# Kernel optimization log

Hardware: AMD Instinct MI355X
Metric: run time of the kernel (lower is better)

Reference implementation:

```python
import jax, jax.numpy as jnp
import numpy as np

N = 4096

def setup_inputs() -> dict:
    key = jax.random.key(0)
    kA, kB = jax.random.split(key)
    A = jnp.tril(jax.random.normal(kA, (N, N), dtype=jnp.float32))
    B = jnp.tril(jax.random.normal(kB, (N, N), dtype=jnp.float32))
    return {"A": A, "B": B}

def reference(A, B):
    # Product of two lower-triangular matrices; result is lower-triangular.
    # tril applied to the dense matmul reproduces the intended math exactly
    # (and zeroes any numerical noise in the structural-zero upper triangle).
    return jnp.tril(jnp.matmul(A, B))
```

## Files before the change

### kernel.cpp

```cpp
#include <hip/hip_runtime.h>
#include <stdint.h>

#define NN 4096
#define NB 32
#define BK 32

#define NHEAVY 136
#define NHUNITS 272
#define ZBASE 664
#define TGRID 1160

#define PGRID 8328

typedef __bf16 bf16x8 __attribute__((ext_vector_type(8)));
typedef float f32x4 __attribute__((ext_vector_type(4)));
typedef unsigned short ushort8 __attribute__((ext_vector_type(8)));

__device__ __forceinline__ unsigned short f2bf(float x) {
    union { float f; unsigned int u; } v; v.f = x;
    unsigned int u = v.u;
    u += 0x7fffu + ((u >> 16) & 1u);
    return (unsigned short)(u >> 16);
}

#define GLOAD16(g, l) __builtin_amdgcn_global_load_lds( \
    (const __attribute__((address_space(1))) unsigned int*)(g), \
    (__attribute__((address_space(3))) unsigned int*)(l), 16, 0, 0)

__device__ __forceinline__ void heavy_map(int h, int& bi, int& bj) {
    int t = h, d = NB - 1;
    while (t >= NB - d) { t -= NB - d; --d; }
    bj = t; bi = t + d;
}

__global__ __launch_bounds__(256) void prep(const float* __restrict__ A,
                                            const float* __restrict__ B,
                                            unsigned short* __restrict__ Ab,
                                            unsigned short* __restrict__ Bt,
                                            float* __restrict__ C) {
    __shared__ float tile[64][65];
    int bid = blockIdx.x;
    int tid = threadIdx.x;

    if (bid < 4096) {
        int i = bid;
        int nslots = (((i >> 7) + 1) * 128) >> 3;
        const float4* src = reinterpret_cast<const float4*>(A + (size_t)i * NN);
        unsigned short* dst = Ab + (size_t)i * NN;
        for (int p = tid; p < nslots; p += 256) {
            float4 x0 = src[p * 2], x1 = src[p * 2 + 1];
            ushort8 o;
            o[0] = f2bf(x0.x); o[1] = f2bf(x0.y); o[2] = f2bf(x0.z); o[3] = f2bf(x0.w);
            o[4] = f2bf(x1.x); o[5] = f2bf(x1.y); o[6] = f2bf(x1.z); o[7] = f2bf(x1.w);
            *reinterpret_cast<ushort8*>(dst + p * 8) = o;
        }
        return;
    }
    if (bid < 8192) {
        int s = bid - 4096;
        int n64 = s >> 6, k64 = s & 63;
        if (k64 < (n64 & ~1)) return;
        int n0 = n64 * 64, k0 = k64 * 64;
        int tx = tid & 63, ty = tid >> 6;
#pragma unroll
        for (int r = 0; r < 16; ++r) {
            int k = ty + r * 4;
            tile[k][tx] = B[(size_t)(k0 + k) * NN + n0 + tx];
        }
        __syncthreads();
#pragma unroll
        for (int r = 0; r < 16; ++r) {
            int n = ty + r * 4;
            Bt[(size_t)(n0 + n) * NN + k0 + tx] = f2bf(tile[tx][n]);
        }
        return;
    }
    int h = bid - 8192;
    int bi, bj; heavy_map(h, bi, bj);
    float4 z = make_float4(0.f, 0.f, 0.f, 0.f);
    float4* cp = reinterpret_cast<float4*>(C + (size_t)bi * 128 * NN + (size_t)bj * 128);
#pragma unroll
    for (int i2 = 0; i2 < 16; ++i2) {
        int slot = tid + i2 * 256;
        int row = slot >> 5, c4 = slot & 31;
        cp[(size_t)row * (NN / 4) + c4] = z;
    }
}

__global__ __launch_bounds__(256) void trimm(const unsigned short* __restrict__ Ab,
                                             const unsigned short* __restrict__ Bt,
                                             float* __restrict__ C) {
    int bid = blockIdx.x;
    int tid = threadIdx.x;
    int lane = tid & 63;
    int w = tid >> 6;

    int bi, bj;
    bool heavy = false;
    int k_lo, k_hi;

    if (bid >= ZBASE) {
        int t = bid - ZBASE;
        int r = 0, cnt = NB - 1;
        while (t >= cnt) { t -= cnt; ++r; --cnt; }
        bi = r; bj = r + 1 + t;
        float4 z = make_float4(0.f, 0.f, 0.f, 0.f);
        float4* cp = reinterpret_cast<float4*>(C + (size_t)bi * 128 * NN + (size_t)bj * 128);
#pragma unroll
        for (int i2 = 0; i2 < 16; ++i2) {
            int slot = tid + i2 * 256;
            int row = slot >> 5, c4 = slot & 31;
            cp[(size_t)row * (NN / 4) + c4] = z;
        }
        return;
    }
    if (bid < NHUNITS) {
        heavy = true;
        int h = bid >> 1, half = bid & 1;
        heavy_map(h, bi, bj);
        k_lo = bj * 128;
        k_hi = (bi + 1) * 128;
        int len = (k_hi - k_lo) >> 1;
        if (half == 0) k_hi = k_lo + len;
        else           k_lo = k_lo + len;
    } else {
        int t = bid - NHUNITS, d = 15;
        while (t >= NB - d) { t -= NB - d; --d; }
        bj = t; bi = t + d;
        k_lo = bj * 128;
        k_hi = (bi + 1) * 128;
    }

    __shared__ unsigned short As[2][128 * BK];
    __shared__ unsigned short Bs[2][128 * BK];

    int wr = w >> 1, wc = w & 1;

    int srow = w * 32 + (lane >> 2);
    int skoff = (lane & 3) * 8;
    const unsigned short* gA0 = Ab + (size_t)(bi * 128 + srow) * NN + skoff;
    const unsigned short* gA1 = gA0 + (size_t)16 * NN;
    const unsigned short* gB0 = Bt + (size_t)(bj * 128 + srow) * NN + skoff;
    const unsigned short* gB1 = gB0 + (size_t)16 * NN;

    f32x4 acc[4][4];
#pragma unroll
    for (int mi = 0; mi < 4; ++mi)
#pragma unroll
        for (int ni = 0; ni < 4; ++ni)
            acc[mi][ni] = (f32x4){0.f, 0.f, 0.f, 0.f};

    int arow = wr * 64 + (lane & 15);
    int brow = wc * 64 + (lane & 15);
    int kq = (lane >> 4) * 8;

    {
        unsigned short* a = &As[0][w * 1024];
        unsigned short* b = &Bs[0][w * 1024];
        GLOAD16(gA0 + k_lo, a);
        GLOAD16(gA1 + k_lo, a + 512);
        GLOAD16(gB0 + k_lo, b);
        GLOAD16(gB1 + k_lo, b + 512);
    }
    int cur = 0;

    for (int kt = k_lo; kt < k_hi; kt += BK) {
        __syncthreads();

        if (kt + BK < k_hi) {
            unsigned short* a = &As[cur ^ 1][w * 1024];
            unsigned short* b = &Bs[cur ^ 1][w * 1024];
            GLOAD16(gA0 + kt + BK, a);
            GLOAD16(gA1 + kt + BK, a + 512);
            GLOAD16(gB0 + kt + BK, b);
            GLOAD16(gB1 + kt + BK, b + 512);
        }

        bf16x8 af[4], bfr[4];
#pragma unroll
        for (int mi = 0; mi < 4; ++mi)
            af[mi] = *reinterpret_cast<const bf16x8*>(&As[cur][(arow + mi * 16) * BK + kq]);
#pragma unroll
        for (int ni = 0; ni < 4; ++ni)
            bfr[ni] = *reinterpret_cast<const bf16x8*>(&Bs[cur][(brow + ni * 16) * BK + kq]);
#pragma unroll
        for (int mi = 0; mi < 4; ++mi)
#pragma unroll
            for (int ni = 0; ni < 4; ++ni)
                acc[mi][ni] = __builtin_amdgcn_mfma_f32_16x16x32_bf16(af[mi], bfr[ni], acc[mi][ni], 0, 0, 0);

        cur ^= 1;
    }

    int crow0 = bi * 128 + wr * 64 + (lane >> 4) * 4;
    int ccol0 = bj * 128 + wc * 64 + (lane & 15);
    if (heavy) {
#pragma unroll
        for (int mi = 0; mi < 4; ++mi)
#pragma unroll
            for (int ni = 0; ni < 4; ++ni) {
                float* cp = C + (size_t)(crow0 + mi * 16) * NN + ccol0 + ni * 16;
#pragma unroll
                for (int r2 = 0; r2 < 4; ++r2)
                    atomicAdd(&cp[(size_t)r2 * NN], acc[mi][ni][r2]);
            }
    } else {
#pragma unroll
        for (int mi = 0; mi < 4; ++mi)
#pragma unroll
            for (int ni = 0; ni < 4; ++ni) {
                float* cp = C + (size_t)(crow0 + mi * 16) * NN + ccol0 + ni * 16;
#pragma unroll
                for (int r2 = 0; r2 < 4; ++r2)
                    cp[(size_t)r2 * NN] = acc[mi][ni][r2];
            }
    }
}

extern "C" void kernel_launch(void* const* d_in, const int* in_sizes, int n_in,
                              void* d_out, int out_size, void* d_ws, size_t ws_size,
                              hipStream_t stream) {
    const float* A = (const float*)d_in[0];
    const float* B = (const float*)d_in[1];
    float* C = (float*)d_out;
    unsigned short* Ab = (unsigned short*)d_ws;
    unsigned short* Bt = Ab + (size_t)NN * NN;
    prep<<<PGRID, 256, 0, stream>>>(A, B, Ab, Bt, C);
    trimm<<<TGRID, 256, 0, stream>>>(Ab, Bt, C);
}
```

Before: 85.86 us.

## Split every lower tile's K range into 512-wide chunks with atomic accumulation

Replaces the two-way split of only the heaviest tiles with a uniform split-K scheme. Each lower-triangular 128x128 output tile's K range is cut into chunks of at most 512, giving 1704 work units of bounded length. Tiles that need several chunks are zeroed in prep and accumulated with atomics, while single-chunk tiles store directly. This evens out per-block work and fills the GPU better, at the cost of many more atomic adds and more zeroing of C in prep.

```diff
diff --git a/kernel.cpp b/kernel.cpp
--- a/kernel.cpp
+++ b/kernel.cpp
@@ -5,12 +5,12 @@
 #define NB 32
 #define BK 32
 
-#define NHEAVY 136
-#define NHUNITS 272
-#define ZBASE 664
-#define TGRID 1160
-
-#define PGRID 8328
+#define NUNITS 1704
+#define ZBASE 1704
+#define TGRID 2200
+
+#define NMULTI 406
+#define PGRID 8598
 
 typedef __bf16 bf16x8 __attribute__((ext_vector_type(8)));
 typedef float f32x4 __attribute__((ext_vector_type(4)));
@@ -26,12 +26,6 @@
 #define GLOAD16(g, l) __builtin_amdgcn_global_load_lds( \
     (const __attribute__((address_space(1))) unsigned int*)(g), \
     (__attribute__((address_space(3))) unsigned int*)(l), 16, 0, 0)
-
-__device__ __forceinline__ void heavy_map(int h, int& bi, int& bj) {
-    int t = h, d = NB - 1;
-    while (t >= NB - d) { t -= NB - d; --d; }
-    bj = t; bi = t + d;
-}
 
 __global__ __launch_bounds__(256) void prep(const float* __restrict__ A,
                                             const float* __restrict__ B,
@@ -75,15 +69,22 @@
         }
         return;
     }
-    int h = bid - 8192;
-    int bi, bj; heavy_map(h, bi, bj);
-    float4 z = make_float4(0.f, 0.f, 0.f, 0.f);
-    float4* cp = reinterpret_cast<float4*>(C + (size_t)bi * 128 * NN + (size_t)bj * 128);
-#pragma unroll
-    for (int i2 = 0; i2 < 16; ++i2) {
-        int slot = tid + i2 * 256;
-        int row = slot >> 5, c4 = slot & 31;
-        cp[(size_t)row * (NN / 4) + c4] = z;
+    {
+        int z = bid - 8192;
+        int d = 31, bi, bj;
+        for (;;) {
+            int cnt = NB - d;
+            if (z < cnt) { bj = z; bi = z + d; break; }
+            z -= cnt; --d;
+        }
+        float4 zf = make_float4(0.f, 0.f, 0.f, 0.f);
+        float4* cp = reinterpret_cast<float4*>(C + (size_t)bi * 128 * NN + (size_t)bj * 128);
+#pragma unroll
+        for (int i2 = 0; i2 < 16; ++i2) {
+            int slot = tid + i2 * 256;
+            int row = slot >> 5, c4 = slot & 31;
+            cp[(size_t)row * (NN / 4) + c4] = zf;
+        }
     }
 }
 
@@ -96,8 +97,8 @@
     int w = tid >> 6;
 
     int bi, bj;
-    bool heavy = false;
     int k_lo, k_hi;
+    bool multi;
 
     if (bid >= ZBASE) {
         int t = bid - ZBASE;
@@ -114,21 +115,21 @@
         }
         return;
     }
-    if (bid < NHUNITS) {
-        heavy = true;
-        int h = bid >> 1, half = bid & 1;
-        heavy_map(h, bi, bj);
-        k_lo = bj * 128;
-        k_hi = (bi + 1) * 128;
-        int len = (k_hi - k_lo) >> 1;
-        if (half == 0) k_hi = k_lo + len;
-        else           k_lo = k_lo + len;
-    } else {
-        int t = bid - NHUNITS, d = 15;
-        while (t >= NB - d) { t -= NB - d; --d; }
+    {
+        int r = bid, d = 31, nu;
+        for (;;) {
+            nu = (d + 4) >> 2;
+            int cnt = (NB - d) * nu;
+            if (r < cnt) break;
+            r -= cnt; --d;
+        }
+        int t = r / nu;
+        int u = r - t * nu;
         bj = t; bi = t + d;
-        k_lo = bj * 128;
-        k_hi = (bi + 1) * 128;
+        multi = (nu > 1);
+        int klt = bj * 128, kht = (bi + 1) * 128;
+        k_lo = klt + u * 512;
+        k_hi = k_lo + 512 < kht ? k_lo + 512 : kht;
     }
 
     __shared__ unsigned short As[2][128 * BK];
@@ -194,7 +195,7 @@
 
     int crow0 = bi * 128 + wr * 64 + (lane >> 4) * 4;
     int ccol0 = bj * 128 + wc * 64 + (lane & 15);
-    if (heavy) {
+    if (multi) {
 #pragma unroll
         for (int mi = 0; mi < 4; ++mi)
 #pragma unroll
```

New measurement: 129.9 us. 51.2% more time.

## Swizzle LDS k-offsets and deepen global-to-LDS prefetch with partial vmcnt waits

Applied to the files above, without the earlier changes.

XOR-swizzles the k-chunk offset used when staging A/B tiles into LDS and when reading MFMA fragments, to spread LDS bank accesses. It also restructures the double-buffered loop so two stages are in flight: the next-next tile is issued right after compute, and a vmcnt(4) wait plus a raw barrier replaces the full __syncthreads. This lets global loads overlap more compute. In exchange, the tail iterations issue redundant loads to keep the wait counts uniform, and the manual waitcnt handling is fragile.

```diff
diff --git a/kernel.cpp b/kernel.cpp
--- a/kernel.cpp
+++ b/kernel.cpp
@@ -5,7 +5,6 @@
 #define NB 32
 #define BK 32
 
-#define NHEAVY 136
 #define NHUNITS 272
 #define ZBASE 664
 #define TGRID 1160
@@ -137,7 +136,7 @@
     int wr = w >> 1, wc = w & 1;
 
     int srow = w * 32 + (lane >> 2);
-    int skoff = (lane & 3) * 8;
+    int skoff = (((lane & 3) ^ ((lane >> 3) & 3)) * 8);
     const unsigned short* gA0 = Ab + (size_t)(bi * 128 + srow) * NN + skoff;
     const unsigned short* gA1 = gA0 + (size_t)16 * NN;
     const unsigned short* gB0 = Bt + (size_t)(bj * 128 + srow) * NN + skoff;
@@ -152,29 +151,27 @@
 
     int arow = wr * 64 + (lane & 15);
     int brow = wc * 64 + (lane & 15);
-    int kq = (lane >> 4) * 8;
-
+    int kq = (((lane >> 4) ^ ((lane >> 1) & 3)) * 8);
+
+#define STAGE(bufsel, kk) do { \
+        unsigned short* a_ = &As[bufsel][w * 1024]; \
+        unsigned short* b_ = &Bs[bufsel][w * 1024]; \
+        GLOAD16(gA0 + (kk), a_); \
+        GLOAD16(gA1 + (kk), a_ + 512); \
+        GLOAD16(gB0 + (kk), b_); \
+        GLOAD16(gB1 + (kk), b_ + 512); \
+    } while (0)
+
+    STAGE(0, k_lo);
     {
-        unsigned short* a = &As[0][w * 1024];
-        unsigned short* b = &Bs[0][w * 1024];
-        GLOAD16(gA0 + k_lo, a);
-        GLOAD16(gA1 + k_lo, a + 512);
-        GLOAD16(gB0 + k_lo, b);
-        GLOAD16(gB1 + k_lo, b + 512);
+        int k1 = (k_lo + BK < k_hi) ? (k_lo + BK) : k_lo;
+        STAGE(1, k1);
     }
     int cur = 0;
 
     for (int kt = k_lo; kt < k_hi; kt += BK) {
-        __syncthreads();
-
-        if (kt + BK < k_hi) {
-            unsigned short* a = &As[cur ^ 1][w * 1024];
-            unsigned short* b = &Bs[cur ^ 1][w * 1024];
-            GLOAD16(gA0 + kt + BK, a);
-            GLOAD16(gA1 + kt + BK, a + 512);
-            GLOAD16(gB0 + kt + BK, b);
-            GLOAD16(gB1 + kt + BK, b + 512);
-        }
+        asm volatile("s_waitcnt vmcnt(4)" ::: "memory");
+        __builtin_amdgcn_s_barrier();
 
         bf16x8 af[4], bfr[4];
 #pragma unroll
@@ -189,8 +186,16 @@
             for (int ni = 0; ni < 4; ++ni)
                 acc[mi][ni] = __builtin_amdgcn_mfma_f32_16x16x32_bf16(af[mi], bfr[ni], acc[mi][ni], 0, 0, 0);
 
+        __builtin_amdgcn_s_barrier();
+
+        int kn = kt + 2 * BK;
+        if (kn >= k_hi) kn = k_lo;
+        STAGE(cur, kn);
+
         cur ^= 1;
     }
+    asm volatile("s_waitcnt vmcnt(0)" ::: "memory");
+#undef STAGE
 
     int crow0 = bi * 128 + wr * 64 + (lane >> 4) * 4;
     int ccol0 = bj * 128 + wc * 64 + (lane & 15);
```

Result: slower. 88.68 us (+3.3%).
